# Performance work log

Hardware: AMD Instinct MI355X
Metric: run time of the kernel (lower is better)

The kernel has to match this reference:

```python
import jax, jax.numpy as jnp
import numpy as np

N, E, B = 50000, 800000, 512
DIN, H, G, M = 128, 128, 32, 128
EPS = 1e-5


def _gcn_layer(h, src, dst, W, b):
    h = h @ W  # [N, H]
    loop = jnp.arange(N)
    s = jnp.concatenate([src, loop])
    d = jnp.concatenate([dst, loop])
    deg = jax.ops.segment_sum(jnp.ones(s.shape, h.dtype), d, num_segments=N)
    dinv = jax.lax.rsqrt(jnp.maximum(deg, 1.0))  # deg >= 1 due to self-loops
    norm = dinv[s] * dinv[d]  # [E+N]
    out = jax.ops.segment_sum(norm[:, None] * h[s], d, num_segments=N)
    return out + b


def _bn_relu(h, gamma, beta):
    mu = jnp.mean(h, axis=0)
    var = jnp.mean((h - mu) ** 2, axis=0)
    return jax.nn.relu((h - mu) * jax.lax.rsqrt(var + EPS) * gamma + beta)


def setup_inputs() -> dict:
    key = jax.random.key(0)
    ks = jax.random.split(key, 20)
    inp = {
        "x": jax.random.normal(ks[0], (N, DIN), jnp.float32),
        "edge_index": jax.random.randint(ks[1], (2, E), 0, N),
        "batch": jnp.sort(jax.random.randint(ks[2], (N,), 0, B)),
        "global_feats": jax.random.normal(ks[3], (B, G), jnp.float32),
    }
    dims = [DIN, H, H]
    for i in range(3):
        inp[f"W{i}"] = jax.random.normal(ks[4 + i], (dims[i], H), jnp.float32) / np.sqrt(dims[i])
        inp[f"b{i}"] = jnp.zeros((H,), jnp.float32)
        inp[f"g{i}"] = jnp.ones((H,), jnp.float32)
        inp[f"be{i}"] = jnp.zeros((H,), jnp.float32)
    inp["M1w"] = jax.random.normal(ks[10], (H + G, M), jnp.float32) / np.sqrt(H + G)
    inp["M1b"] = jnp.zeros((M,), jnp.float32)
    inp["M2w"] = jax.random.normal(ks[11], (M, M // 2), jnp.float32) / np.sqrt(M)
    inp["M2b"] = jnp.zeros((M // 2,), jnp.float32)
    inp["M3w"] = jax.random.normal(ks[12], (M // 2, 1), jnp.float32) / np.sqrt(M // 2)
    inp["M3b"] = jnp.zeros((1,), jnp.float32)
    return inp


def reference(x, edge_index, batch, global_feats,
              W0, b0, g0, be0, W1, b1, g1, be1, W2, b2, g2, be2,
              M1w, M1b, M2w, M2b, M3w, M3b):
    src, dst = edge_index[0], edge_index[1]
    h = x
    for W, b, g, be in ((W0, b0, g0, be0), (W1, b1, g1, be1), (W2, b2, g2, be2)):
        h = _bn_relu(_gcn_layer(h, src, dst, W, b), g, be)
    # global mean pool over graphs
    sums = jax.ops.segment_sum(h, batch, num_segments=B)  # [B, H]
    cnt = jax.ops.segment_sum(jnp.ones((N,), h.dtype), batch, num_segments=B)
    pooled = sums / jnp.maximum(cnt, 1.0)[:, None]
    z = jnp.concatenate([pooled, global_feats], axis=1)  # [B, H+G]
    z = jax.nn.relu(z @ M1w + M1b)
    z = jax.nn.relu(z @ M2w + M2b)
    out = z @ M3w + M3b  # [B, 1]
    return out.reshape(-1)
```

## Files before the change

kernel.cpp:

```cpp
#include <hip/hip_runtime.h>

#define NN 50000
#define NE 800000
#define BG 512
#define HD 128
#define GD 32
#define MD 128
#define EPSV 1e-5f
#define NBK 256
#define BSTR 196
#define BCAP 4096
#define SP 136
#define CSB 128

typedef __attribute__((ext_vector_type(8))) short bf16x8;
typedef __attribute__((ext_vector_type(4))) float f32x4;

static __device__ __forceinline__ unsigned short f2bf(float f) {
    unsigned int u = __float_as_uint(f);
    u += 0x7fffu + ((u >> 16) & 1u);
    return (unsigned short)(u >> 16);
}
static __device__ __forceinline__ float bfu(unsigned short v) {
    return __uint_as_float((unsigned int)v << 16);
}
static __device__ __forceinline__ float bf_lo(unsigned int v) {
    return __uint_as_float(v << 16);
}
static __device__ __forceinline__ float bf_hi(unsigned int v) {
    return __uint_as_float(v & 0xffff0000u);
}

__global__ __launch_bounds__(256) void k_bin(const int* __restrict__ src,
                                             const int* __restrict__ dst,
                                             int* __restrict__ bucket_cnt,
                                             unsigned int* __restrict__ binned) {
    __shared__ int hcnt[NBK];
    __shared__ int hbase[NBK];
    int tid = threadIdx.x;
    int e0 = blockIdx.x * 2048;
    unsigned int pv[8];
    int bk[8], rk[8];
#pragma unroll
    for (int i = 0; i < 8; ++i) {
        int e = e0 + i * 256 + tid;
        if (e < NE) {
            int s = src[e];
            int d = dst[e];
            bk[i] = d / BSTR;
            pv[i] = ((unsigned int)(d - bk[i] * BSTR) << 16) | (unsigned int)s;
        } else {
            bk[i] = -1;
        }
    }
    hcnt[tid] = 0;
    __syncthreads();
#pragma unroll
    for (int i = 0; i < 8; ++i)
        if (bk[i] >= 0) rk[i] = atomicAdd(&hcnt[bk[i]], 1);
    __syncthreads();
    hbase[tid] = atomicAdd(&bucket_cnt[tid], hcnt[tid]);
    __syncthreads();
#pragma unroll
    for (int i = 0; i < 8; ++i)
        if (bk[i] >= 0)
            binned[(size_t)bk[i] * BCAP + hbase[bk[i]] + rk[i]] = pv[i];
}

__global__ __launch_bounds__(256) void k_csr(const unsigned int* __restrict__ binned,
                                             const int* __restrict__ bucket_cnt,
                                             int* __restrict__ offsets,
                                             float* __restrict__ dinv,
                                             int* __restrict__ csr,
                                             const float* __restrict__ W0,
                                             const float* __restrict__ W1,
                                             const float* __restrict__ W2,
                                             unsigned short* __restrict__ Wt) {
    __shared__ unsigned short sW[128 * 130];
    __shared__ int ls[256];
    __shared__ int h[BSTR];
    __shared__ int cur[BSTR];
    __shared__ int bpre_s;
    int b = blockIdx.x, t = threadIdx.x;
    if (b >= NBK) {
        const float* Wsrc = (b == NBK) ? W0 : ((b == NBK + 1) ? W1 : W2);
#pragma unroll
        for (int i = 0; i < 64; ++i) {
            int idx = i * 256 + t;
            int k = idx >> 7, n = idx & 127;
            sW[n * 130 + k] = f2bf(Wsrc[idx]);
        }
        __syncthreads();
        unsigned short* o = Wt + (size_t)(b - NBK) * 16384;
#pragma unroll
        for (int i = 0; i < 64; ++i) {
            int idx = i * 256 + t;
            int n = idx >> 7, k = idx & 127;
            o[idx] = sW[n * 130 + k];
        }
        return;
    }
    int bc = bucket_cnt[t];
    ls[t] = bc;
    __syncthreads();
    for (int off = 1; off < 256; off <<= 1) {
        int c0 = ls[t];
        int add = (t >= off) ? ls[t - off] : 0;
        __syncthreads();
        ls[t] = c0 + add;
        __syncthreads();
    }
    if (t == b) bpre_s = ls[t] - bc;
    if (t < BSTR) h[t] = 0;
    __syncthreads();
    int bpre = bpre_s;
    int nb = bucket_cnt[b];
    const unsigned int* base = binned + (size_t)b * BCAP;
    for (int e = t; e < nb; e += 256)
        atomicAdd(&h[base[e] >> 16], 1);
    __syncthreads();
    int c = (t < BSTR) ? h[t] : 0;
    ls[t] = c;
    __syncthreads();
    for (int off = 1; off < 256; off <<= 1) {
        int c0 = ls[t];
        int add = (t >= off) ? ls[t - off] : 0;
        __syncthreads();
        ls[t] = c0 + add;
        __syncthreads();
    }
    int node = b * BSTR + t;
    if (t < BSTR) {
        int excl = ls[t] - c + bpre;
        cur[t] = excl;
        if (node < NN) {
            offsets[node] = excl;
            dinv[node] = rsqrtf((float)(c + 1));
            if (node == NN - 1) offsets[NN] = NE;
        }
    }
    __syncthreads();
    for (int e = t; e < nb; e += 256) {
        unsigned int v = base[e];
        int pos = atomicAdd(&cur[v >> 16], 1);
        csr[pos] = (int)(v & 0xffffu);
    }
}

__global__ __launch_bounds__(256) void k_gemm(const float* __restrict__ Inf,
                                              const unsigned short* __restrict__ Inh,
                                              const unsigned short* __restrict__ Wt,
                                              unsigned short* __restrict__ Th,
                                              const float* __restrict__ pstats,
                                              const float* __restrict__ gamma,
                                              const float* __restrict__ beta,
                                              const float* __restrict__ dinv,
                                              int useBN) {
    __shared__ unsigned short Abf[64 * SP];
    __shared__ unsigned short WtL[128 * SP];
    __shared__ float ssS[256];
    int tid = threadIdx.x;
    int rowBase = blockIdx.x * 64;
    if (useBN) {
        float a = 0.f;
#pragma unroll 4
        for (int b = 0; b < CSB; ++b) a += pstats[b * 256 + tid];
        ssS[tid] = a;
        __syncthreads();
        if (tid < 128) {
            float mu = ssS[tid] * (1.f / NN);
            float var = ssS[128 + tid] * (1.f / NN) - mu * mu;
            float sc = gamma[tid] * rsqrtf(var + EPSV);
            float sh = beta[tid] - mu * sc;
            ssS[tid] = sc;
            ssS[128 + tid] = sh;
        }
        __syncthreads();
#pragma unroll
        for (int i = 0; i < 4; ++i) {
            int q = tid + i * 256;
            int row = q >> 4;
            int k8 = (q & 15) * 8;
            int rg = rowBase + row;
            if (rg >= NN) rg = NN - 1;
            bf16x8 raw = *(const bf16x8*)&Inh[(size_t)rg * HD + k8];
            unsigned short o[8];
#pragma unroll
            for (int e = 0; e < 8; ++e) {
                float v = bfu((unsigned short)raw[e]);
                v = fmaxf(v * ssS[k8 + e] + ssS[128 + k8 + e], 0.f);
                o[e] = f2bf(v);
            }
            *(bf16x8*)&Abf[row * SP + k8] = *(bf16x8*)o;
        }
    } else {
#pragma unroll
        for (int i = 0; i < 8; ++i) {
            int q = tid + i * 256;
            int row = q >> 5;
            int c4 = (q & 31) * 4;
            int rg = rowBase + row;
            if (rg >= NN) rg = NN - 1;
            float4 v = *(const float4*)&Inf[(size_t)rg * HD + c4];
            unsigned short* p = &Abf[row * SP + c4];
            p[0] = f2bf(v.x); p[1] = f2bf(v.y); p[2] = f2bf(v.z); p[3] = f2bf(v.w);
        }
    }
#pragma unroll
    for (int i = 0; i < 8; ++i) {
        int q = tid + i * 256;
        int n = q >> 4;
        int k8 = (q & 15) * 8;
        bf16x8 w = *(const bf16x8*)&Wt[n * HD + k8];
        *(bf16x8*)&WtL[n * SP + k8] = w;
    }
    __syncthreads();
    int lane = tid & 63;
    int wv = tid >> 6;
    int quad = lane >> 4;
    int lrow = wv * 16 + (lane & 15);
    f32x4 acc[8];
#pragma unroll
    for (int c = 0; c < 8; ++c) acc[c] = (f32x4){0.f, 0.f, 0.f, 0.f};
#pragma unroll
    for (int qk = 0; qk < 4; ++qk) {
        int ko = quad * 8 + qk * 32;
        bf16x8 bfr = *(const bf16x8*)&Abf[lrow * SP + ko];
#pragma unroll
        for (int c = 0; c < 8; ++c) {
            bf16x8 afr = *(const bf16x8*)&WtL[(c * 16 + (lane & 15)) * SP + ko];
            acc[c] = __builtin_amdgcn_mfma_f32_16x16x32_bf16(afr, bfr, acc[c], 0, 0, 0);
        }
    }
    int grow = rowBase + lrow;
    if (grow < NN) {
        float di = dinv[grow];
#pragma unroll
        for (int c = 0; c < 8; ++c) {
            ushort4 o;
            o.x = f2bf(acc[c][0] * di);
            o.y = f2bf(acc[c][1] * di);
            o.z = f2bf(acc[c][2] * di);
            o.w = f2bf(acc[c][3] * di);
            *(ushort4*)&Th[(size_t)grow * HD + c * 16 + quad * 4] = o;
        }
    }
}

__global__ __launch_bounds__(256, 8) void k_aggregate(const uint2* __restrict__ T2,
                                                      const int* __restrict__ offsets,
                                                      const int* __restrict__ csr,
                                                      const float* __restrict__ dinv,
                                                      const float* __restrict__ bias,
                                                      unsigned short* __restrict__ Ah) {
    int d = blockIdx.x * 4 + (threadIdx.x >> 6);
    int l = threadIdx.x & 63;
    int half = l >> 5;
    int li = l & 31;
    if (d >= NN) return;
    int start = offsets[d], end = offsets[d + 1];
    float a0 = 0.f, a1 = 0.f, a2 = 0.f, a3 = 0.f;
    int j = start;
    for (; j + 15 < end; j += 16) {
        int s[8];
        uint2 v[8];
#pragma unroll
        for (int i = 0; i < 8; ++i) s[i] = csr[j + 2 * i + half];
#pragma unroll
        for (int i = 0; i < 8; ++i) v[i] = T2[(size_t)s[i] * 32 + li];
#pragma unroll
        for (int i = 0; i < 8; ++i) {
            a0 += bf_lo(v[i].x); a1 += bf_hi(v[i].x);
            a2 += bf_lo(v[i].y); a3 += bf_hi(v[i].y);
        }
    }
    for (; j + 7 < end; j += 8) {
        int s0 = csr[j + half];
        int s1 = csr[j + 2 + half];
        int s2 = csr[j + 4 + half];
        int s3 = csr[j + 6 + half];
        uint2 v0 = T2[(size_t)s0 * 32 + li];
        uint2 v1 = T2[(size_t)s1 * 32 + li];
        uint2 v2 = T2[(size_t)s2 * 32 + li];
        uint2 v3 = T2[(size_t)s3 * 32 + li];
        a0 += bf_lo(v0.x); a1 += bf_hi(v0.x); a2 += bf_lo(v0.y); a3 += bf_hi(v0.y);
        a0 += bf_lo(v1.x); a1 += bf_hi(v1.x); a2 += bf_lo(v1.y); a3 += bf_hi(v1.y);
        a0 += bf_lo(v2.x); a1 += bf_hi(v2.x); a2 += bf_lo(v2.y); a3 += bf_hi(v2.y);
        a0 += bf_lo(v3.x); a1 += bf_hi(v3.x); a2 += bf_lo(v3.y); a3 += bf_hi(v3.y);
    }
    for (; j + 1 < end; j += 2) {
        int s0 = csr[j + half];
        uint2 v0 = T2[(size_t)s0 * 32 + li];
        a0 += bf_lo(v0.x); a1 += bf_hi(v0.x); a2 += bf_lo(v0.y); a3 += bf_hi(v0.y);
    }
    if (j < end && half == 0) {
        int s0 = csr[j];
        uint2 v0 = T2[(size_t)s0 * 32 + li];
        a0 += bf_lo(v0.x); a1 += bf_hi(v0.x); a2 += bf_lo(v0.y); a3 += bf_hi(v0.y);
    }
    a0 += __shfl_xor(a0, 32);
    a1 += __shfl_xor(a1, 32);
    a2 += __shfl_xor(a2, 32);
    a3 += __shfl_xor(a3, 32);
    if (half == 0) {
        float di = dinv[d];
        uint2 vd = T2[(size_t)d * 32 + li];
        float4 bs = *(const float4*)&bias[4 * li];
        ushort4 o;
        o.x = f2bf(di * (a0 + bf_lo(vd.x)) + bs.x);
        o.y = f2bf(di * (a1 + bf_hi(vd.x)) + bs.y);
        o.z = f2bf(di * (a2 + bf_lo(vd.y)) + bs.z);
        o.w = f2bf(di * (a3 + bf_hi(vd.y)) + bs.w);
        *(ushort4*)&Ah[(size_t)d * HD + 4 * li] = o;
    }
}

__global__ __launch_bounds__(256) void k_colstats(const uint2* __restrict__ A2,
                                                  float* __restrict__ pstats) {
    int li = threadIdx.x & 31;
    int rr = threadIdx.x >> 5;
    float4 s = {0.f, 0.f, 0.f, 0.f}, q = {0.f, 0.f, 0.f, 0.f};
    for (int row = blockIdx.x * 8 + rr; row < NN; row += CSB * 8) {
        uint2 u = A2[(size_t)row * 32 + li];
        float x0 = bf_lo(u.x), x1 = bf_hi(u.x), x2 = bf_lo(u.y), x3 = bf_hi(u.y);
        s.x += x0; s.y += x1; s.z += x2; s.w += x3;
        q.x += x0 * x0; q.y += x1 * x1; q.z += x2 * x2; q.w += x3 * x3;
    }
    __shared__ float4 lsum[256], lqum[256];
    lsum[threadIdx.x] = s;
    lqum[threadIdx.x] = q;
    __syncthreads();
    if (rr == 0) {
        float4 a = lsum[li];
#pragma unroll
        for (int g = 1; g < 8; ++g) {
            float4 b = lsum[g * 32 + li];
            a.x += b.x; a.y += b.y; a.z += b.z; a.w += b.w;
        }
        *(float4*)&pstats[blockIdx.x * 256 + 4 * li] = a;
    } else if (rr == 1) {
        float4 a = lqum[li];
#pragma unroll
        for (int g = 1; g < 8; ++g) {
            float4 b = lqum[g * 32 + li];
            a.x += b.x; a.y += b.y; a.z += b.z; a.w += b.w;
        }
        *(float4*)&pstats[blockIdx.x * 256 + 128 + 4 * li] = a;
    }
}

__global__ __launch_bounds__(256) void k_bnfinal(const float* __restrict__ pstats,
                                                 const float* __restrict__ gamma,
                                                 const float* __restrict__ beta,
                                                 float* __restrict__ ss) {
    __shared__ float sums[256];
    int t = threadIdx.x;
    float a = 0.f;
#pragma unroll 4
    for (int b = 0; b < CSB; ++b) a += pstats[b * 256 + t];
    sums[t] = a;
    __syncthreads();
    if (t < 128) {
        float mu = sums[t] * (1.f / NN);
        float var = sums[128 + t] * (1.f / NN) - mu * mu;
        float sc = gamma[t] * rsqrtf(var + EPSV);
        ss[t] = sc;
        ss[128 + t] = beta[t] - mu * sc;
    }
}

__global__ __launch_bounds__(256) void k_pool(const unsigned int* __restrict__ Au,
                                              const int* __restrict__ batch,
                                              const float* __restrict__ ss,
                                              float* __restrict__ pooled) {
    int t = threadIdx.x;
    int fu = t & 63;
    int half = t >> 6;
    int r0 = blockIdx.x * 64;
    int rend = min(r0 + 64, NN);
    float s0 = ss[2 * fu], s1 = ss[2 * fu + 1];
    float h0 = ss[128 + 2 * fu], h1 = ss[128 + 2 * fu + 1];
    float a0 = 0.f, a1 = 0.f;
    int cg = -1;
    for (int r = r0 + half; r < rend; r += 4) {
        int g = batch[r];
        if (g != cg) {
            if (cg >= 0) {
                atomicAdd(&pooled[(size_t)cg * HD + 2 * fu], a0);
                atomicAdd(&pooled[(size_t)cg * HD + 2 * fu + 1], a1);
            }
            cg = g;
            a0 = 0.f; a1 = 0.f;
        }
        unsigned int v = Au[(size_t)r * 64 + fu];
        a0 += fmaxf(bf_lo(v) * s0 + h0, 0.f);
        a1 += fmaxf(bf_hi(v) * s1 + h1, 0.f);
    }
    if (cg >= 0) {
        atomicAdd(&pooled[(size_t)cg * HD + 2 * fu], a0);
        atomicAdd(&pooled[(size_t)cg * HD + 2 * fu + 1], a1);
    }
}

__global__ __launch_bounds__(128) void k_mlp(const float* __restrict__ pooled,
                                             const int* __restrict__ batch,
                                             const float* __restrict__ gfeat,
                                             const float* __restrict__ M1w,
                                             const float* __restrict__ M1b,
                                             const float* __restrict__ M2w,
                                             const float* __restrict__ M2b,
                                             const float* __restrict__ M3w,
                                             const float* __restrict__ M3b,
                                             float* __restrict__ out) {
    __shared__ int sb[2];
    __shared__ float z[HD + GD];
    __shared__ float z1[MD];
    __shared__ float z2[MD / 2];
    int b = blockIdx.x, t = threadIdx.x;
    if (t < 2) {
        int val = b + t;
        int lo = 0, hi = NN;
        while (lo < hi) {
            int mid = (lo + hi) >> 1;
            if (batch[mid] < val) lo = mid + 1; else hi = mid;
        }
        sb[t] = lo;
    }
    __syncthreads();
    float ic = 1.f / fmaxf((float)(sb[1] - sb[0]), 1.f);
    z[t] = pooled[(size_t)b * HD + t] * ic;
    if (t < GD) z[HD + t] = gfeat[b * GD + t];
    __syncthreads();
    float a = M1b[t];
    for (int k = 0; k < HD + GD; ++k) a += z[k] * M1w[k * MD + t];
    z1[t] = fmaxf(a, 0.f);
    __syncthreads();
    if (t < MD / 2) {
        float a2 = M2b[t];
        for (int k = 0; k < MD; ++k) a2 += z1[k] * M2w[k * (MD / 2) + t];
        z2[t] = fmaxf(a2, 0.f);
    }
    __syncthreads();
    if (t < 64) {
        float p = z2[t] * M3w[t];
#pragma unroll
        for (int off = 32; off; off >>= 1) p += __shfl_down(p, off);
        if (t == 0) out[b] = p + M3b[0];
    }
}

static inline size_t alg(size_t x) { return (x + 255) & ~(size_t)255; }

extern "C" void kernel_launch(void* const* d_in, const int* in_sizes, int n_in,
                              void* d_out, int out_size, void* d_ws, size_t ws_size,
                              hipStream_t stream) {
    const float* x = (const float*)d_in[0];
    const int* ei = (const int*)d_in[1];
    const int* batch = (const int*)d_in[2];
    const float* gf = (const float*)d_in[3];
    const float* W[3] = {(const float*)d_in[4], (const float*)d_in[8], (const float*)d_in[12]};
    const float* bb[3] = {(const float*)d_in[5], (const float*)d_in[9], (const float*)d_in[13]};
    const float* gg[3] = {(const float*)d_in[6], (const float*)d_in[10], (const float*)d_in[14]};
    const float* be[3] = {(const float*)d_in[7], (const float*)d_in[11], (const float*)d_in[15]};
    const float* M1w = (const float*)d_in[16];
    const float* M1b = (const float*)d_in[17];
    const float* M2w = (const float*)d_in[18];
    const float* M2b = (const float*)d_in[19];
    const float* M3w = (const float*)d_in[20];
    const float* M3b = (const float*)d_in[21];
    float* out = (float*)d_out;

    char* w = (char*)d_ws;
    int* bucket_cnt = (int*)w;    w += alg((size_t)NBK * 4);
    float* pooled = (float*)w;    w += alg((size_t)BG * HD * 4);
    size_t zspan = (size_t)(w - (char*)d_ws);
    int* offsets = (int*)w;       w += alg((size_t)(NN + 1) * 4);
    int* csr = (int*)w;           w += alg((size_t)NE * 4);
    float* dinv = (float*)w;      w += alg((size_t)NN * 4);
    float* pstats = (float*)w;    w += alg((size_t)CSB * 256 * 4);
    float* ss = (float*)w;        w += alg(256 * 4);
    unsigned short* Wt = (unsigned short*)w;  w += alg((size_t)3 * 16384 * 2);
    unsigned int* binned = (unsigned int*)w;  w += alg((size_t)NBK * BCAP * 4);
    unsigned short* Ah = (unsigned short*)w;  w += alg((size_t)NN * HD * 2);
    unsigned short* Th = (unsigned short*)w;  w += alg((size_t)NN * HD * 2);

    const int* src = ei;
    const int* dst = ei + NE;

    hipMemsetAsync(bucket_cnt, 0, zspan, stream);
    k_bin<<<(NE + 2047) / 2048, 256, 0, stream>>>(src, dst, bucket_cnt, binned);
    k_csr<<<NBK + 3, 256, 0, stream>>>(binned, bucket_cnt, offsets, dinv, csr,
                                       W[0], W[1], W[2], Wt);

    for (int L = 0; L < 3; ++L) {
        k_gemm<<<(NN + 63) / 64, 256, 0, stream>>>(x, Ah, Wt + (size_t)L * 16384, Th,
                                                   pstats, gg[L ? L - 1 : 0],
                                                   be[L ? L - 1 : 0], dinv, L > 0);
        k_aggregate<<<(NN + 3) / 4, 256, 0, stream>>>((const uint2*)Th, offsets, csr,
                                                      dinv, bb[L], Ah);
        k_colstats<<<CSB, 256, 0, stream>>>((const uint2*)Ah, pstats);
    }
    k_bnfinal<<<1, 256, 0, stream>>>(pstats, gg[2], be[2], ss);

    k_pool<<<(NN + 63) / 64, 256, 0, stream>>>((const unsigned int*)Ah, batch, ss, pooled);
    k_mlp<<<BG, 128, 0, stream>>>(pooled, batch, gf, M1w, M1b, M2w, M2b, M3w, M3b, out);
}
```

Measured before the change: 377.2 us.

## Drop GEMM LDS staging, atomically reduce BN stats, fold bnfinal into pool

The GEMM no longer stages the activation tile and the transposed weights in shared memory. Each lane loads its own A fragment straight from global memory (applying BN+ReLU or the fp32-to-bf16 conversion in registers), and the weight fragments are read directly from the global Wt buffer. Column statistics are now accumulated with atomics into a per-layer 256-float buffer that is zeroed by the existing memset, so every GEMM block reads 256 floats instead of reducing 128x256 partials. The separate k_bnfinal launch is removed and its scale/shift math is recomputed in each k_pool block. In exchange, weight reads now go through L1/L2 without LDS reuse, and float atomics make the statistics order-nondeterministic.

```diff
diff --git a/kernel.cpp b/kernel.cpp
--- a/kernel.cpp
+++ b/kernel.cpp
@@ -10,7 +10,6 @@
 #define NBK 256
 #define BSTR 196
 #define BCAP 4096
-#define SP 136
 #define CSB 128
 
 typedef __attribute__((ext_vector_type(8))) short bf16x8;
@@ -151,21 +150,16 @@
                                               const unsigned short* __restrict__ Inh,
                                               const unsigned short* __restrict__ Wt,
                                               unsigned short* __restrict__ Th,
-                                              const float* __restrict__ pstats,
+                                              const float* __restrict__ stats,
                                               const float* __restrict__ gamma,
                                               const float* __restrict__ beta,
                                               const float* __restrict__ dinv,
                                               int useBN) {
-    __shared__ unsigned short Abf[64 * SP];
-    __shared__ unsigned short WtL[128 * SP];
     __shared__ float ssS[256];
     int tid = threadIdx.x;
     int rowBase = blockIdx.x * 64;
     if (useBN) {
-        float a = 0.f;
-#pragma unroll 4
-        for (int b = 0; b < CSB; ++b) a += pstats[b * 256 + tid];
-        ssS[tid] = a;
+        ssS[tid] = stats[tid];
         __syncthreads();
         if (tid < 128) {
             float mu = ssS[tid] * (1.f / NN);
@@ -176,63 +170,43 @@
             ssS[128 + tid] = sh;
         }
         __syncthreads();
-#pragma unroll
-        for (int i = 0; i < 4; ++i) {
-            int q = tid + i * 256;
-            int row = q >> 4;
-            int k8 = (q & 15) * 8;
-            int rg = rowBase + row;
-            if (rg >= NN) rg = NN - 1;
-            bf16x8 raw = *(const bf16x8*)&Inh[(size_t)rg * HD + k8];
-            unsigned short o[8];
+    }
+    int lane = tid & 63;
+    int wv = tid >> 6;
+    int m = lane & 15;
+    int quad = lane >> 4;
+    int lrow = wv * 16 + m;
+    int grow = rowBase + lrow;
+    int gr = (grow < NN) ? grow : NN - 1;
+    f32x4 acc[8];
+#pragma unroll
+    for (int c = 0; c < 8; ++c) acc[c] = (f32x4){0.f, 0.f, 0.f, 0.f};
+#pragma unroll
+    for (int qk = 0; qk < 4; ++qk) {
+        int ko = quad * 8 + qk * 32;
+        bf16x8 bfr;
+        unsigned short ob[8];
+        if (useBN) {
+            bf16x8 raw = *(const bf16x8*)&Inh[(size_t)gr * HD + ko];
 #pragma unroll
             for (int e = 0; e < 8; ++e) {
                 float v = bfu((unsigned short)raw[e]);
-                v = fmaxf(v * ssS[k8 + e] + ssS[128 + k8 + e], 0.f);
-                o[e] = f2bf(v);
+                v = fmaxf(v * ssS[ko + e] + ssS[128 + ko + e], 0.f);
+                ob[e] = f2bf(v);
             }
-            *(bf16x8*)&Abf[row * SP + k8] = *(bf16x8*)o;
-        }
-    } else {
-#pragma unroll
-        for (int i = 0; i < 8; ++i) {
-            int q = tid + i * 256;
-            int row = q >> 5;
-            int c4 = (q & 31) * 4;
-            int rg = rowBase + row;
-            if (rg >= NN) rg = NN - 1;
-            float4 v = *(const float4*)&Inf[(size_t)rg * HD + c4];
-            unsigned short* p = &Abf[row * SP + c4];
-            p[0] = f2bf(v.x); p[1] = f2bf(v.y); p[2] = f2bf(v.z); p[3] = f2bf(v.w);
-        }
-    }
-#pragma unroll
-    for (int i = 0; i < 8; ++i) {
-        int q = tid + i * 256;
-        int n = q >> 4;
-        int k8 = (q & 15) * 8;
-        bf16x8 w = *(const bf16x8*)&Wt[n * HD + k8];
-        *(bf16x8*)&WtL[n * SP + k8] = w;
-    }
-    __syncthreads();
-    int lane = tid & 63;
-    int wv = tid >> 6;
-    int quad = lane >> 4;
-    int lrow = wv * 16 + (lane & 15);
-    f32x4 acc[8];
-#pragma unroll
-    for (int c = 0; c < 8; ++c) acc[c] = (f32x4){0.f, 0.f, 0.f, 0.f};
-#pragma unroll
-    for (int qk = 0; qk < 4; ++qk) {
-        int ko = quad * 8 + qk * 32;
-        bf16x8 bfr = *(const bf16x8*)&Abf[lrow * SP + ko];
+        } else {
+            float4 a = *(const float4*)&Inf[(size_t)gr * HD + ko];
+            float4 b = *(const float4*)&Inf[(size_t)gr * HD + ko + 4];
+            ob[0] = f2bf(a.x); ob[1] = f2bf(a.y); ob[2] = f2bf(a.z); ob[3] = f2bf(a.w);
+            ob[4] = f2bf(b.x); ob[5] = f2bf(b.y); ob[6] = f2bf(b.z); ob[7] = f2bf(b.w);
+        }
+        bfr = *(bf16x8*)ob;
 #pragma unroll
         for (int c = 0; c < 8; ++c) {
-            bf16x8 afr = *(const bf16x8*)&WtL[(c * 16 + (lane & 15)) * SP + ko];
+            bf16x8 afr = *(const bf16x8*)&Wt[(size_t)(c * 16 + m) * HD + ko];
             acc[c] = __builtin_amdgcn_mfma_f32_16x16x32_bf16(afr, bfr, acc[c], 0, 0, 0);
         }
     }
-    int grow = rowBase + lrow;
     if (grow < NN) {
         float di = dinv[grow];
 #pragma unroll
@@ -316,7 +290,7 @@
 }
 
 __global__ __launch_bounds__(256) void k_colstats(const uint2* __restrict__ A2,
-                                                  float* __restrict__ pstats) {
+                                                  float* __restrict__ stats) {
     int li = threadIdx.x & 31;
     int rr = threadIdx.x >> 5;
     float4 s = {0.f, 0.f, 0.f, 0.f}, q = {0.f, 0.f, 0.f, 0.f};
@@ -337,7 +311,10 @@
             float4 b = lsum[g * 32 + li];
             a.x += b.x; a.y += b.y; a.z += b.z; a.w += b.w;
         }
-        *(float4*)&pstats[blockIdx.x * 256 + 4 * li] = a;
+        atomicAdd(&stats[4 * li + 0], a.x);
+        atomicAdd(&stats[4 * li + 1], a.y);
+        atomicAdd(&stats[4 * li + 2], a.z);
+        atomicAdd(&stats[4 * li + 3], a.w);
     } else if (rr == 1) {
         float4 a = lqum[li];
 #pragma unroll
@@ -345,41 +322,38 @@
             float4 b = lqum[g * 32 + li];
             a.x += b.x; a.y += b.y; a.z += b.z; a.w += b.w;
         }
-        *(float4*)&pstats[blockIdx.x * 256 + 128 + 4 * li] = a;
-    }
-}
-
-__global__ __launch_bounds__(256) void k_bnfinal(const float* __restrict__ pstats,
-                                                 const float* __restrict__ gamma,
-                                                 const float* __restrict__ beta,
-                                                 float* __restrict__ ss) {
-    __shared__ float sums[256];
-    int t = threadIdx.x;
-    float a = 0.f;
-#pragma unroll 4
-    for (int b = 0; b < CSB; ++b) a += pstats[b * 256 + t];
-    sums[t] = a;
-    __syncthreads();
-    if (t < 128) {
-        float mu = sums[t] * (1.f / NN);
-        float var = sums[128 + t] * (1.f / NN) - mu * mu;
-        float sc = gamma[t] * rsqrtf(var + EPSV);
-        ss[t] = sc;
-        ss[128 + t] = beta[t] - mu * sc;
+        atomicAdd(&stats[128 + 4 * li + 0], a.x);
+        atomicAdd(&stats[128 + 4 * li + 1], a.y);
+        atomicAdd(&stats[128 + 4 * li + 2], a.z);
+        atomicAdd(&stats[128 + 4 * li + 3], a.w);
     }
 }
 
 __global__ __launch_bounds__(256) void k_pool(const unsigned int* __restrict__ Au,
                                               const int* __restrict__ batch,
-                                              const float* __restrict__ ss,
+                                              const float* __restrict__ stats,
+                                              const float* __restrict__ gamma,
+                                              const float* __restrict__ beta,
                                               float* __restrict__ pooled) {
+    __shared__ float ssP[256];
     int t = threadIdx.x;
+    ssP[t] = stats[t];
+    __syncthreads();
+    if (t < 128) {
+        float mu = ssP[t] * (1.f / NN);
+        float var = ssP[128 + t] * (1.f / NN) - mu * mu;
+        float sc = gamma[t] * rsqrtf(var + EPSV);
+        float sh = beta[t] - mu * sc;
+        ssP[t] = sc;
+        ssP[128 + t] = sh;
+    }
+    __syncthreads();
     int fu = t & 63;
     int half = t >> 6;
     int r0 = blockIdx.x * 64;
     int rend = min(r0 + 64, NN);
-    float s0 = ss[2 * fu], s1 = ss[2 * fu + 1];
-    float h0 = ss[128 + 2 * fu], h1 = ss[128 + 2 * fu + 1];
+    float s0 = ssP[2 * fu], s1 = ssP[2 * fu + 1];
+    float h0 = ssP[128 + 2 * fu], h1 = ssP[128 + 2 * fu + 1];
     float a0 = 0.f, a1 = 0.f;
     int cg = -1;
     for (int r = r0 + half; r < rend; r += 4) {
@@ -473,12 +447,11 @@
     char* w = (char*)d_ws;
     int* bucket_cnt = (int*)w;    w += alg((size_t)NBK * 4);
     float* pooled = (float*)w;    w += alg((size_t)BG * HD * 4);
+    float* stats = (float*)w;     w += alg((size_t)3 * 256 * 4);
     size_t zspan = (size_t)(w - (char*)d_ws);
     int* offsets = (int*)w;       w += alg((size_t)(NN + 1) * 4);
     int* csr = (int*)w;           w += alg((size_t)NE * 4);
     float* dinv = (float*)w;      w += alg((size_t)NN * 4);
-    float* pstats = (float*)w;    w += alg((size_t)CSB * 256 * 4);
-    float* ss = (float*)w;        w += alg(256 * 4);
     unsigned short* Wt = (unsigned short*)w;  w += alg((size_t)3 * 16384 * 2);
     unsigned int* binned = (unsigned int*)w;  w += alg((size_t)NBK * BCAP * 4);
     unsigned short* Ah = (unsigned short*)w;  w += alg((size_t)NN * HD * 2);
@@ -494,14 +467,15 @@
 
     for (int L = 0; L < 3; ++L) {
         k_gemm<<<(NN + 63) / 64, 256, 0, stream>>>(x, Ah, Wt + (size_t)L * 16384, Th,
-                                                   pstats, gg[L ? L - 1 : 0],
-                                                   be[L ? L - 1 : 0], dinv, L > 0);
+                                                   stats + (L ? (L - 1) * 256 : 0),
+                                                   gg[L ? L - 1 : 0], be[L ? L - 1 : 0],
+                                                   dinv, L > 0);
         k_aggregate<<<(NN + 3) / 4, 256, 0, stream>>>((const uint2*)Th, offsets, csr,
                                                       dinv, bb[L], Ah);
-        k_colstats<<<CSB, 256, 0, stream>>>((const uint2*)Ah, pstats);
-    }
-    k_bnfinal<<<1, 256, 0, stream>>>(pstats, gg[2], be[2], ss);
-
-    k_pool<<<(NN + 63) / 64, 256, 0, stream>>>((const unsigned int*)Ah, batch, ss, pooled);
+        k_colstats<<<CSB, 256, 0, stream>>>((const uint2*)Ah, stats + L * 256);
+    }
+
+    k_pool<<<(NN + 63) / 64, 256, 0, stream>>>((const unsigned int*)Ah, batch,
+                                               stats + 2 * 256, gg[2], be[2], pooled);
     k_mlp<<<BG, 128, 0, stream>>>(pooled, batch, gf, M1w, M1b, M2w, M2b, M3w, M3b, out);
 }
```

Measured after the change: 403.4 us. 1.07x slower.
